# Kernel optimization log

Measured on AMD Instinct MI355X. Metric: run time of the kernel, lower is better.

The kernel has to match this reference:

```python
import jax, jax.numpy as jnp
import numpy as np

N_EMBD = 2048
N_HEAD = 16
N_KV_HEAD = 4
HD = N_EMBD // N_HEAD  # 128
B, T = 1, 4096
EPS = 1e-6


def apply_rope(x, cos, sin):
    # x: [B,T,H,hd]; cos/sin: [T,1,hd//2]
    hd = x.shape[-1] // 2
    x1, x2 = x[..., :hd], x[..., hd:]
    y1 = x1 * cos + x2 * sin
    y2 = x2 * cos - x1 * sin
    return jnp.concatenate((y1, y2), axis=-1).astype(x.dtype)


def rms_norm(x, eps=EPS):
    return x * jax.lax.rsqrt(jnp.mean(jnp.square(x), axis=-1, keepdims=True) + eps)


def setup_inputs() -> dict:
    key = jax.random.key(0)
    ks = jax.random.split(key, 7)
    s = 0.02
    return {
        "x": jax.random.normal(ks[0], (B, T, N_EMBD), dtype=jnp.float32),
        "cos": jax.random.normal(ks[1], (T, 1, HD // 2), dtype=jnp.float32),
        "sin": jax.random.normal(ks[2], (T, 1, HD // 2), dtype=jnp.float32),
        "wq": jax.random.normal(ks[3], (N_EMBD, N_HEAD * HD), dtype=jnp.float32) * s,
        "wk": jax.random.normal(ks[4], (N_EMBD, N_KV_HEAD * HD), dtype=jnp.float32) * s,
        "wv": jax.random.normal(ks[5], (N_EMBD, N_KV_HEAD * HD), dtype=jnp.float32) * s,
        "wo": jax.random.normal(ks[6], (N_EMBD, N_EMBD), dtype=jnp.float32) * s,
    }


def reference(x, cos, sin, wq, wk, wv, wo):
    Bb, Tt, C = x.shape
    q = (x @ wq).reshape(Bb, Tt, N_HEAD, HD)
    k = (x @ wk).reshape(Bb, Tt, N_KV_HEAD, HD)
    v = (x @ wv).reshape(Bb, Tt, N_KV_HEAD, HD)
    q = rms_norm(apply_rope(q, cos, sin))
    k = rms_norm(apply_rope(k, cos, sin))
    g = N_HEAD // N_KV_HEAD
    if g > 1:
        k = jnp.repeat(k, g, axis=2)  # [B,T,H,hd]
        v = jnp.repeat(v, g, axis=2)
    scale = 1.0 / jnp.sqrt(jnp.float32(HD))
    # scores: [B,H,T,S]
    scores = jnp.einsum("bthd,bshd->bhts", q, k) * scale
    causal = jnp.tril(jnp.ones((Tt, Tt), dtype=bool))
    scores = jnp.where(causal, scores, jnp.finfo(scores.dtype).min)
    attn = jax.nn.softmax(scores, axis=-1)
    y = jnp.einsum("bhts,bshd->bthd", attn, v).reshape(Bb, Tt, C)
    return y @ wo
```

## Files before the change

kernel.cpp:

```cpp
#include <hip/hip_runtime.h>

#define T_SEQ 4096
#define C_EMB 2048
#define NH 16
#define NKV 4
#define HD 128

typedef short bf16x8 __attribute__((ext_vector_type(8)));
typedef float f32x4 __attribute__((ext_vector_type(4)));
typedef unsigned short u16x4 __attribute__((ext_vector_type(4)));

__device__ inline unsigned short f2bf(float f) {
    unsigned int u = __float_as_uint(f);
    unsigned int r = (u + 0x7FFFu + ((u >> 16) & 1u)) >> 16;
    return (unsigned short)r;
}

__device__ __forceinline__ void async_cp16(const unsigned short* g, unsigned short* l) {
    __builtin_amdgcn_global_load_lds((const __attribute__((address_space(1))) unsigned int*)g,
                                     (__attribute__((address_space(3))) unsigned int*)l,
                                     16, 0, 0);
}

__global__ __launch_bounds__(256) void cvt_bf16(const float* __restrict__ in,
                                                unsigned short* __restrict__ out, int n) {
    int i = (blockIdx.x * 256 + threadIdx.x) * 4;
    if (i >= n) return;
    float4 f = *(const float4*)(&in[i]);
    u16x4 o;
    o.x = f2bf(f.x); o.y = f2bf(f.y); o.z = f2bf(f.z); o.w = f2bf(f.w);
    *(u16x4*)(&out[i]) = o;
}

__global__ __launch_bounds__(256) void transpose_all(const float* __restrict__ wq,
                                                     const float* __restrict__ wk,
                                                     const float* __restrict__ wv,
                                                     const float* __restrict__ wo,
                                                     unsigned short* __restrict__ wqkvT,
                                                     unsigned short* __restrict__ woT) {
    __shared__ float tile[32][33];
    int z = blockIdx.z;
    const float* in;
    unsigned short* out;
    int ld_in;
    if (z == 0)      { in = wq; out = wqkvT;                         ld_in = 2048; }
    else if (z == 1) { in = wk; out = wqkvT + (size_t)2048 * 2048;   ld_in = 512;  }
    else if (z == 2) { in = wv; out = wqkvT + (size_t)2560 * 2048;   ld_in = 512;  }
    else             { in = wo; out = woT;                           ld_in = 2048; }
    if ((z == 1 || z == 2) && blockIdx.x >= 16) return;

    int x = blockIdx.x * 32 + threadIdx.x;
    for (int i = threadIdx.y; i < 32; i += 8) {
        int y = blockIdx.y * 32 + i;
        tile[i][threadIdx.x] = in[(size_t)y * ld_in + x];
    }
    __syncthreads();
    int xo = blockIdx.y * 32 + threadIdx.x;
    for (int i = threadIdx.y; i < 32; i += 8) {
        int yo = blockIdx.x * 32 + i;
        out[(size_t)yo * 2048 + xo] = f2bf(tile[threadIdx.x][i]);
    }
}

__global__ __launch_bounds__(256, 3) void gemm_qkv(const unsigned short* __restrict__ A,
                                                   const unsigned short* __restrict__ Bt,
                                                   const float* __restrict__ cosb,
                                                   const float* __restrict__ sinb,
                                                   unsigned short* __restrict__ Qn,
                                                   unsigned short* __restrict__ Kn,
                                                   unsigned short* __restrict__ Vt) {
    __shared__ __align__(16) unsigned short As[3][128 * 32];
    __shared__ __align__(16) unsigned short Bs[3][128 * 32];
    const int K = 2048;
    int t = threadIdx.x;
    int w = t >> 6, lane = t & 63;
    int ln = lane & 15, q = lane >> 4;
    int wm = w * 32;

    int d = blockIdx.y * 24 + blockIdx.x;
    int xcd = d & 7, l = d >> 3;
    int lx = l % 12, ly = l / 12;
    int bx = (xcd & 1) * 12 + lx;
    int by = (xcd >> 1) * 8 + ly;
    int m0 = by * 128, n0 = bx * 128;

    f32x4 acc[2][8] = {};

    int r0 = t >> 2, c0 = (t & 3) ^ ((t >> 4) & 3);
    int L1 = 256 + t;
    int r1 = L1 >> 2, c1 = (L1 & 3) ^ ((L1 >> 4) & 3);
    const unsigned short* a0 = &A[(size_t)(m0 + r0) * K + c0 * 8];
    const unsigned short* a1 = &A[(size_t)(m0 + r1) * K + c1 * 8];
    const unsigned short* b0 = &Bt[(size_t)(n0 + r0) * K + c0 * 8];
    const unsigned short* b1 = &Bt[(size_t)(n0 + r1) * K + c1 * 8];

    auto stage = [&](int b, int k0) {
        async_cp16(a0 + k0, &As[b][w * 512]);
        async_cp16(a1 + k0, &As[b][2048 + w * 512]);
        async_cp16(b0 + k0, &Bs[b][w * 512]);
        async_cp16(b1 + k0, &Bs[b][2048 + w * 512]);
    };

    stage(0, 0);
    stage(1, 32);

    int bc = 0;
    for (int it = 0; it < 64; ++it) {
        if (it < 63) asm volatile("s_waitcnt vmcnt(4)" ::: "memory");
        else         asm volatile("s_waitcnt vmcnt(0)" ::: "memory");
        __builtin_amdgcn_s_barrier();
        __builtin_amdgcn_sched_barrier(0);
        if (it < 62) {
            int bn = bc + 2; if (bn >= 3) bn -= 3;
            stage(bn, (it + 2) * 32);
        }
        int cs = (q ^ ((ln >> 2) & 3)) * 8;
        bf16x8 af[2], bfr[8];
#pragma unroll
        for (int i = 0; i < 2; ++i) af[i] = *(const bf16x8*)(&As[bc][(wm + i * 16 + ln) * 32 + cs]);
#pragma unroll
        for (int j = 0; j < 8; ++j) bfr[j] = *(const bf16x8*)(&Bs[bc][(j * 16 + ln) * 32 + cs]);
#pragma unroll
        for (int i = 0; i < 2; ++i)
#pragma unroll
            for (int j = 0; j < 8; ++j)
                acc[i][j] = __builtin_amdgcn_mfma_f32_16x16x32_bf16(af[i], bfr[j], acc[i][j], 0, 0, 0);
        bc = (bc == 2) ? 0 : bc + 1;
    }

    if (n0 < 2560) {
        bool isQ = (n0 < 2048);
        int h = isQ ? (n0 >> 7) : ((n0 - 2048) >> 7);
#pragma unroll
        for (int i = 0; i < 2; ++i)
#pragma unroll
            for (int r = 0; r < 4; ++r) {
                int row = m0 + wm + i * 16 + q * 4 + r;
                float y1[4], y2[4];
                float ss = 0.0f;
#pragma unroll
                for (int j = 0; j < 4; ++j) {
                    float a = acc[i][j][r];
                    float b = acc[i][j + 4][r];
                    float cc = cosb[row * 64 + j * 16 + ln];
                    float sv = sinb[row * 64 + j * 16 + ln];
                    y1[j] = a * cc + b * sv;
                    y2[j] = b * cc - a * sv;
                    ss += y1[j] * y1[j] + y2[j] * y2[j];
                }
                ss += __shfl_xor(ss, 1);
                ss += __shfl_xor(ss, 2);
                ss += __shfl_xor(ss, 4);
                ss += __shfl_xor(ss, 8);
                float rv = rsqrtf(ss * (1.0f / 128.0f) + 1e-6f);
                if (isQ) {
                    float s = rv * (0.08838834764831845f * 1.4426950408889634f);
                    unsigned short* ob = Qn + (size_t)row * 2048 + h * 128;
#pragma unroll
                    for (int j = 0; j < 4; ++j) {
                        ob[j * 16 + ln] = f2bf(y1[j] * s);
                        ob[64 + j * 16 + ln] = f2bf(y2[j] * s);
                    }
                } else {
                    unsigned short* ob = Kn + (size_t)row * 512 + h * 128;
#pragma unroll
                    for (int j = 0; j < 4; ++j) {
                        ob[j * 16 + ln] = f2bf(y1[j] * rv);
                        ob[64 + j * 16 + ln] = f2bf(y2[j] * rv);
                    }
                }
            }
    } else {
        int v0 = n0 - 2560;
        unsigned short* sm = &As[0][0];
#pragma unroll
        for (int half = 0; half < 2; ++half) {
            __syncthreads();
#pragma unroll
            for (int i = 0; i < 2; ++i)
#pragma unroll
                for (int jj = 0; jj < 4; ++jj) {
                    int j = half * 4 + jj;
                    int cc = jj * 16 + ln;
                    int rr = wm + i * 16 + q * 4;
                    u16x4 pk;
                    pk.x = f2bf(acc[i][j][0]); pk.y = f2bf(acc[i][j][1]);
                    pk.z = f2bf(acc[i][j][2]); pk.w = f2bf(acc[i][j][3]);
                    *(u16x4*)(&sm[cc * 136 + rr]) = pk;
                }
            __syncthreads();
            int vtr = t >> 2, mseg = (t & 3) * 32;
            unsigned short* dst = Vt + (size_t)(v0 + half * 64 + vtr) * 4096 + m0 + mseg;
            const unsigned short* src = &sm[vtr * 136 + mseg];
            *(int4*)(dst)      = *(const int4*)(src);
            *(int4*)(dst + 8)  = *(const int4*)(src + 8);
            *(int4*)(dst + 16) = *(const int4*)(src + 16);
            *(int4*)(dst + 24) = *(const int4*)(src + 24);
        }
    }
}

__global__ __launch_bounds__(512, 2) void gemm_bt_256(const unsigned short* __restrict__ A,
                                                      const unsigned short* __restrict__ Bt,
                                                      float* __restrict__ C, int M, int N, int K) {
    __shared__ __align__(16) unsigned short As[2][256 * 64];
    __shared__ __align__(16) unsigned short Bs[2][256 * 64];
    int t = threadIdx.x;
    int w = t >> 6, lane = t & 63;
    int ln = lane & 15, q = lane >> 4;
    int wr = w >> 2, wc = w & 3;
    int m0 = blockIdx.y * 256, n0 = blockIdx.x * 256;

    f32x4 acc[8][4] = {};

    const unsigned short* ab[4];
    const unsigned short* bb[4];
#pragma unroll
    for (int s = 0; s < 4; ++s) {
        int L = s * 512 + t;
        int r = L >> 3;
        int c = (L & 7) ^ (r & 7);
        ab[s] = &A[(size_t)(m0 + r) * K + c * 8];
        bb[s] = &Bt[(size_t)(n0 + r) * K + c * 8];
    }

    auto stage = [&](int b, int k0) {
#pragma unroll
        for (int s = 0; s < 4; ++s) {
            async_cp16(ab[s] + k0, &As[b][s * 4096 + w * 512]);
            async_cp16(bb[s] + k0, &Bs[b][s * 4096 + w * 512]);
        }
    };

    stage(0, 0);
    asm volatile("s_waitcnt vmcnt(0)" ::: "memory");
    __builtin_amdgcn_s_barrier();

    int buf = 0;
    for (int it = 0; it < 32; ++it) {
        if (it < 31) stage(buf ^ 1, (it + 1) * 64);
#pragma unroll
        for (int kk = 0; kk < 2; ++kk) {
            bf16x8 bfr[4];
#pragma unroll
            for (int j = 0; j < 4; ++j) {
                int row = wc * 64 + j * 16 + ln;
                bfr[j] = *(const bf16x8*)(&Bs[buf][row * 64 + (((kk * 4 + q) ^ (row & 7)) * 8)]);
            }
#pragma unroll
            for (int i = 0; i < 8; ++i) {
                int row = wr * 128 + i * 16 + ln;
                bf16x8 a = *(const bf16x8*)(&As[buf][row * 64 + (((kk * 4 + q) ^ (row & 7)) * 8)]);
#pragma unroll
                for (int j = 0; j < 4; ++j)
                    acc[i][j] = __builtin_amdgcn_mfma_f32_16x16x32_bf16(a, bfr[j], acc[i][j], 0, 0, 0);
            }
        }
        asm volatile("s_waitcnt vmcnt(0)" ::: "memory");
        __builtin_amdgcn_s_barrier();
        buf ^= 1;
    }

#pragma unroll
    for (int i = 0; i < 8; ++i)
#pragma unroll
        for (int j = 0; j < 4; ++j)
#pragma unroll
            for (int r = 0; r < 4; ++r) {
                int row = m0 + wr * 128 + i * 16 + q * 4 + r;
                int col = n0 + wc * 64 + j * 16 + ln;
                C[(size_t)row * N + col] = acc[i][j][r];
            }
}

__global__ __launch_bounds__(256) void flash_attn(const unsigned short* __restrict__ Qn,
                                                  const unsigned short* __restrict__ Kn,
                                                  const unsigned short* __restrict__ Vt,
                                                  unsigned short* __restrict__ Ao) {
    __shared__ __align__(16) unsigned short Ks[2][64 * 128];
    __shared__ __align__(16) unsigned short Vs[2][128 * 64];
    __shared__ __align__(16) unsigned short Pl[4][16 * 72];

    int pairi = blockIdx.x;
    int h = blockIdx.y;
    int kvh = h >> 2;
    int t = threadIdx.x;
    int w = t >> 6, lane = t & 63;
    int ln = lane & 15, q = lane >> 4;

    int nA = 64 - pairi;
    int bq = 63 - pairi;
    int wq0 = bq * 64 + w * 16;

    bf16x8 qf[4];
    {
        const unsigned short* qb = Qn + (size_t)(wq0 + ln) * 2048 + h * 128;
#pragma unroll
        for (int kc = 0; kc < 4; ++kc) qf[kc] = *(const bf16x8*)(qb + kc * 32 + q * 8);
    }

    f32x4 o[8] = {};
    f32x4 l_p = {0.f, 0.f, 0.f, 0.f};

    const unsigned short* kbase[4];
    const unsigned short* vbase[4];
#pragma unroll
    for (int s = 0; s < 4; ++s) {
        int L = s * 256 + t;
        int key = L >> 4;
        int ck = (L & 15) ^ (key & 15);
        kbase[s] = Kn + (size_t)key * 512 + kvh * 128 + ck * 8;
        int hd = L >> 3;
        int cv = (L & 7) ^ (hd & 7);
        vbase[s] = Vt + (size_t)(kvh * 128 + hd) * 4096 + cv * 8;
    }

#pragma unroll
    for (int s = 0; s < 4; ++s) async_cp16(kbase[s], &Ks[0][s * 2048 + w * 512]);
#pragma unroll
    for (int s = 0; s < 4; ++s) async_cp16(vbase[s], &Vs[0][s * 2048 + w * 512]);

    for (int it = 0; it < 65; ++it) {
        __syncthreads();

        int nxt = it + 1;
        if (nxt < 65) {
            int nkt = (nxt < nA) ? nxt * 64 : (nxt - nA) * 64;
            size_t koff = (size_t)nkt * 512;
            unsigned short* kd = Ks[nxt & 1];
            unsigned short* vd = Vs[nxt & 1];
#pragma unroll
            for (int s = 0; s < 4; ++s) async_cp16(kbase[s] + koff, kd + s * 2048 + w * 512);
#pragma unroll
            for (int s = 0; s < 4; ++s) async_cp16(vbase[s] + nkt, vd + s * 2048 + w * 512);
        }

        if (it == nA) {
#pragma unroll
            for (int r = 0; r < 4; ++r) {
                float lsum = l_p[r];
                lsum += __shfl_xor(lsum, 1);
                lsum += __shfl_xor(lsum, 2);
                lsum += __shfl_xor(lsum, 4);
                lsum += __shfl_xor(lsum, 8);
                float inv = 1.0f / lsum;
                int row = wq0 + q * 4 + r;
                unsigned short* ob = Ao + (size_t)row * 2048 + h * 128;
#pragma unroll
                for (int f = 0; f < 8; ++f) ob[f * 16 + ln] = f2bf(o[f][r] * inv);
            }
            bq = pairi;
            wq0 = bq * 64 + w * 16;
            const unsigned short* qb = Qn + (size_t)(wq0 + ln) * 2048 + h * 128;
#pragma unroll
            for (int kc = 0; kc < 4; ++kc) qf[kc] = *(const bf16x8*)(qb + kc * 32 + q * 8);
#pragma unroll
            for (int f = 0; f < 8; ++f) o[f] = (f32x4){0.f, 0.f, 0.f, 0.f};
            l_p = (f32x4){0.f, 0.f, 0.f, 0.f};
        }

        int kt0 = (it < nA) ? it * 64 : (it - nA) * 64;
        const unsigned short* kb = Ks[it & 1];
        const unsigned short* vb = Vs[it & 1];

        f32x4 sA[4] = {{-16.6f, -16.6f, -16.6f, -16.6f}, {-16.6f, -16.6f, -16.6f, -16.6f},
                       {-16.6f, -16.6f, -16.6f, -16.6f}, {-16.6f, -16.6f, -16.6f, -16.6f}};
        __builtin_amdgcn_s_setprio(1);
#pragma unroll
        for (int jt = 0; jt < 4; ++jt) {
            int key = jt * 16 + ln;
#pragma unroll
            for (int kc = 0; kc < 4; ++kc) {
                int cs = ((kc * 4 + q) ^ ln) * 8;
                bf16x8 kf = *(const bf16x8*)(&kb[key * 128 + cs]);
                sA[jt] = __builtin_amdgcn_mfma_f32_16x16x32_bf16(qf[kc], kf, sA[jt], 0, 0, 0);
            }
        }
        __builtin_amdgcn_s_setprio(0);
        if (kt0 + 63 > wq0) {
#pragma unroll
            for (int jt = 0; jt < 4; ++jt)
#pragma unroll
                for (int r = 0; r < 4; ++r) {
                    int key = kt0 + jt * 16 + ln;
                    int row = wq0 + q * 4 + r;
                    if (key > row) sA[jt][r] = -3e38f;
                }
        }
#pragma unroll
        for (int r = 0; r < 4; ++r) {
            int prow = (q * 4 + r) * 72;
#pragma unroll
            for (int jt = 0; jt < 4; ++jt) {
                float p = __builtin_amdgcn_exp2f(sA[jt][r]);
                Pl[w][prow + jt * 16 + ln] = (unsigned short)(__float_as_uint(p) >> 16);
                l_p[r] += p;
            }
        }

        __builtin_amdgcn_s_setprio(1);
#pragma unroll
        for (int ks = 0; ks < 2; ++ks) {
            bf16x8 pa = *(const bf16x8*)(&Pl[w][ln * 72 + ks * 32 + q * 8]);
            int cs = ((ks * 4 + q) ^ (ln & 7)) * 8;
#pragma unroll
            for (int f = 0; f < 8; ++f) {
                bf16x8 vf = *(const bf16x8*)(&vb[(f * 16 + ln) * 64 + cs]);
                o[f] = __builtin_amdgcn_mfma_f32_16x16x32_bf16(pa, vf, o[f], 0, 0, 0);
            }
        }
        __builtin_amdgcn_s_setprio(0);
    }
#pragma unroll
    for (int r = 0; r < 4; ++r) {
        float lsum = l_p[r];
        lsum += __shfl_xor(lsum, 1);
        lsum += __shfl_xor(lsum, 2);
        lsum += __shfl_xor(lsum, 4);
        lsum += __shfl_xor(lsum, 8);
        float inv = 1.0f / lsum;
        int row = wq0 + q * 4 + r;
        unsigned short* ob = Ao + (size_t)row * 2048 + h * 128;
#pragma unroll
        for (int f = 0; f < 8; ++f) ob[f * 16 + ln] = f2bf(o[f][r] * inv);
    }
}

extern "C" void kernel_launch(void* const* d_in, const int* in_sizes, int n_in,
                              void* d_out, int out_size, void* d_ws, size_t ws_size,
                              hipStream_t stream) {
    const float* x    = (const float*)d_in[0];
    const float* cosb = (const float*)d_in[1];
    const float* sinb = (const float*)d_in[2];
    const float* wq   = (const float*)d_in[3];
    const float* wk   = (const float*)d_in[4];
    const float* wv   = (const float*)d_in[5];
    const float* wo   = (const float*)d_in[6];
    float* out = (float*)d_out;

    char* ws = (char*)d_ws;
    unsigned short* xb    = (unsigned short*)ws;
    unsigned short* wqkvT = xb    + (size_t)4096 * 2048;
    unsigned short* woT   = wqkvT + (size_t)3072 * 2048;
    unsigned short* Qn    = woT   + (size_t)2048 * 2048;
    unsigned short* Kn    = Qn    + (size_t)4096 * 2048;
    unsigned short* Vt    = Kn    + (size_t)4096 * 512;
    unsigned short* Ao    = Vt    + (size_t)512 * 4096;

    cvt_bf16<<<(4096 * 2048 / 4 + 255) / 256, 256, 0, stream>>>(x, xb, 4096 * 2048);
    transpose_all<<<dim3(64, 64, 4), dim3(32, 8), 0, stream>>>(wq, wk, wv, wo, wqkvT, woT);
    gemm_qkv<<<dim3(24, 32), 256, 0, stream>>>(xb, wqkvT, cosb, sinb, Qn, Kn, Vt);
    flash_attn<<<dim3(32, 16), 256, 0, stream>>>(Qn, Kn, Vt, Ao);
    gemm_bt_256<<<dim3(8, 16), 512, 0, stream>>>(Ao, woT, out, 4096, 2048, 2048);
}
```

Before: 371.9 us.

## Restructure output projection GEMM into triple-buffered phased pipeline with smaller M tile

The output-projection GEMM drops from 256x256 to 128x256 tiles, doubling the grid from 128 to 256 blocks so more CUs are occupied. It replaces double buffering with a 3-stage LDS ring that prefetches two k-steps ahead. Each k-step is split into four MFMA phases, with async loads interleaved and s_setprio raised around the MFMA bursts. The cost is extra barriers per iteration and more total operand traffic from the smaller M tile. The vmcnt(6) counting also has to match the number of outstanding loads exactly.

```diff
diff --git a/kernel.cpp b/kernel.cpp
--- a/kernel.cpp
+++ b/kernel.cpp
@@ -200,74 +200,141 @@
     }
 }
 
-__global__ __launch_bounds__(512, 2) void gemm_bt_256(const unsigned short* __restrict__ A,
+__global__ __launch_bounds__(512, 2) void gemm_bt_8ph(const unsigned short* __restrict__ A,
                                                       const unsigned short* __restrict__ Bt,
                                                       float* __restrict__ C, int M, int N, int K) {
-    __shared__ __align__(16) unsigned short As[2][256 * 64];
-    __shared__ __align__(16) unsigned short Bs[2][256 * 64];
+    __shared__ __align__(16) unsigned short As[3][128 * 64];
+    __shared__ __align__(16) unsigned short Bs[3][256 * 64];
     int t = threadIdx.x;
     int w = t >> 6, lane = t & 63;
     int ln = lane & 15, q = lane >> 4;
     int wr = w >> 2, wc = w & 3;
-    int m0 = blockIdx.y * 256, n0 = blockIdx.x * 256;
-
-    f32x4 acc[8][4] = {};
-
-    const unsigned short* ab[4];
+    int m0 = blockIdx.y * 128, n0 = blockIdx.x * 256;
+
+    f32x4 acc[4][4] = {};
+
+    const unsigned short* ab[2];
     const unsigned short* bb[4];
+#pragma unroll
+    for (int s = 0; s < 2; ++s) {
+        int L = s * 512 + t;
+        int r = L >> 3, c = (L & 7) ^ (r & 7);
+        ab[s] = &A[(size_t)(m0 + r) * K + c * 8];
+    }
 #pragma unroll
     for (int s = 0; s < 4; ++s) {
         int L = s * 512 + t;
-        int r = L >> 3;
-        int c = (L & 7) ^ (r & 7);
-        ab[s] = &A[(size_t)(m0 + r) * K + c * 8];
+        int r = L >> 3, c = (L & 7) ^ (r & 7);
         bb[s] = &Bt[(size_t)(n0 + r) * K + c * 8];
     }
 
-    auto stage = [&](int b, int k0) {
-#pragma unroll
-        for (int s = 0; s < 4; ++s) {
-            async_cp16(ab[s] + k0, &As[b][s * 4096 + w * 512]);
-            async_cp16(bb[s] + k0, &Bs[b][s * 4096 + w * 512]);
-        }
+    auto stageA = [&](int b, int k0) {
+        async_cp16(ab[0] + k0, &As[b][w * 512]);
+        async_cp16(ab[1] + k0, &As[b][4096 + w * 512]);
     };
-
-    stage(0, 0);
-    asm volatile("s_waitcnt vmcnt(0)" ::: "memory");
-    __builtin_amdgcn_s_barrier();
-
-    int buf = 0;
+    auto stageB01 = [&](int b, int k0) {
+        async_cp16(bb[0] + k0, &Bs[b][w * 512]);
+        async_cp16(bb[1] + k0, &Bs[b][4096 + w * 512]);
+    };
+    auto stageB23 = [&](int b, int k0) {
+        async_cp16(bb[2] + k0, &Bs[b][8192 + w * 512]);
+        async_cp16(bb[3] + k0, &Bs[b][12288 + w * 512]);
+    };
+
+    stageA(0, 0); stageB01(0, 0); stageB23(0, 0);
+    stageA(1, 64); stageB01(1, 64); stageB23(1, 64);
+
+    int bc = 0;
     for (int it = 0; it < 32; ++it) {
-        if (it < 31) stage(buf ^ 1, (it + 1) * 64);
-#pragma unroll
-        for (int kk = 0; kk < 2; ++kk) {
-            bf16x8 bfr[4];
-#pragma unroll
-            for (int j = 0; j < 4; ++j) {
-                int row = wc * 64 + j * 16 + ln;
-                bfr[j] = *(const bf16x8*)(&Bs[buf][row * 64 + (((kk * 4 + q) ^ (row & 7)) * 8)]);
-            }
-#pragma unroll
-            for (int i = 0; i < 8; ++i) {
-                int row = wr * 128 + i * 16 + ln;
-                bf16x8 a = *(const bf16x8*)(&As[buf][row * 64 + (((kk * 4 + q) ^ (row & 7)) * 8)]);
-#pragma unroll
-                for (int j = 0; j < 4; ++j)
-                    acc[i][j] = __builtin_amdgcn_mfma_f32_16x16x32_bf16(a, bfr[j], acc[i][j], 0, 0, 0);
-            }
-        }
-        asm volatile("s_waitcnt vmcnt(0)" ::: "memory");
+        if (it < 31) asm volatile("s_waitcnt vmcnt(6)" ::: "memory");
+        else         asm volatile("s_waitcnt vmcnt(0)" ::: "memory");
         __builtin_amdgcn_s_barrier();
-        buf ^= 1;
-    }
-
-#pragma unroll
-    for (int i = 0; i < 8; ++i)
+
+        int bn = bc + 2; if (bn >= 3) bn -= 3;
+        int kn = (it + 2) * 64;
+        bool doStage = (it < 30);
+        const unsigned short* as = &As[bc][0];
+        const unsigned short* bs = &Bs[bc][0];
+        bf16x8 af[4], bfr[4];
+
+#pragma unroll
+        for (int i = 0; i < 4; ++i) {
+            int row = wr * 64 + i * 16 + ln;
+            af[i] = *(const bf16x8*)(&as[row * 64 + ((q ^ (row & 7)) * 8)]);
+        }
+#pragma unroll
+        for (int j = 0; j < 2; ++j) {
+            int row = wc * 64 + j * 16 + ln;
+            bfr[j] = *(const bf16x8*)(&bs[row * 64 + ((q ^ (row & 7)) * 8)]);
+        }
+        if (doStage) stageA(bn, kn);
+        __builtin_amdgcn_s_setprio(1);
+#pragma unroll
+        for (int i = 0; i < 4; ++i)
+#pragma unroll
+            for (int j = 0; j < 2; ++j)
+                acc[i][j] = __builtin_amdgcn_mfma_f32_16x16x32_bf16(af[i], bfr[j], acc[i][j], 0, 0, 0);
+        __builtin_amdgcn_s_setprio(0);
+        __builtin_amdgcn_s_barrier();
+
+#pragma unroll
+        for (int j = 2; j < 4; ++j) {
+            int row = wc * 64 + j * 16 + ln;
+            bfr[j] = *(const bf16x8*)(&bs[row * 64 + ((q ^ (row & 7)) * 8)]);
+        }
+        if (doStage) stageB01(bn, kn);
+        __builtin_amdgcn_s_setprio(1);
+#pragma unroll
+        for (int i = 0; i < 4; ++i)
+#pragma unroll
+            for (int j = 2; j < 4; ++j)
+                acc[i][j] = __builtin_amdgcn_mfma_f32_16x16x32_bf16(af[i], bfr[j], acc[i][j], 0, 0, 0);
+        __builtin_amdgcn_s_setprio(0);
+        __builtin_amdgcn_s_barrier();
+
+#pragma unroll
+        for (int i = 0; i < 4; ++i) {
+            int row = wr * 64 + i * 16 + ln;
+            af[i] = *(const bf16x8*)(&as[row * 64 + (((4 + q) ^ (row & 7)) * 8)]);
+        }
+#pragma unroll
+        for (int j = 0; j < 2; ++j) {
+            int row = wc * 64 + j * 16 + ln;
+            bfr[j] = *(const bf16x8*)(&bs[row * 64 + (((4 + q) ^ (row & 7)) * 8)]);
+        }
+        if (doStage) stageB23(bn, kn);
+        __builtin_amdgcn_s_setprio(1);
+#pragma unroll
+        for (int i = 0; i < 4; ++i)
+#pragma unroll
+            for (int j = 0; j < 2; ++j)
+                acc[i][j] = __builtin_amdgcn_mfma_f32_16x16x32_bf16(af[i], bfr[j], acc[i][j], 0, 0, 0);
+        __builtin_amdgcn_s_setprio(0);
+        __builtin_amdgcn_s_barrier();
+
+#pragma unroll
+        for (int j = 2; j < 4; ++j) {
+            int row = wc * 64 + j * 16 + ln;
+            bfr[j] = *(const bf16x8*)(&bs[row * 64 + (((4 + q) ^ (row & 7)) * 8)]);
+        }
+        __builtin_amdgcn_s_setprio(1);
+#pragma unroll
+        for (int i = 0; i < 4; ++i)
+#pragma unroll
+            for (int j = 2; j < 4; ++j)
+                acc[i][j] = __builtin_amdgcn_mfma_f32_16x16x32_bf16(af[i], bfr[j], acc[i][j], 0, 0, 0);
+        __builtin_amdgcn_s_setprio(0);
+
+        bc = (bc == 2) ? 0 : bc + 1;
+    }
+
+#pragma unroll
+    for (int i = 0; i < 4; ++i)
 #pragma unroll
         for (int j = 0; j < 4; ++j)
 #pragma unroll
             for (int r = 0; r < 4; ++r) {
-                int row = m0 + wr * 128 + i * 16 + q * 4 + r;
+                int row = m0 + wr * 64 + i * 16 + q * 4 + r;
                 int col = n0 + wc * 64 + j * 16 + ln;
                 C[(size_t)row * N + col] = acc[i][j][r];
             }
@@ -451,5 +518,5 @@
     transpose_all<<<dim3(64, 64, 4), dim3(32, 8), 0, stream>>>(wq, wk, wv, wo, wqkvT, woT);
     gemm_qkv<<<dim3(24, 32), 256, 0, stream>>>(xb, wqkvT, cosb, sinb, Qn, Kn, Vt);
     flash_attn<<<dim3(32, 16), 256, 0, stream>>>(Qn, Kn, Vt, Ao);
-    gemm_bt_256<<<dim3(8, 16), 512, 0, stream>>>(Ao, woT, out, 4096, 2048, 2048);
-}
+    gemm_bt_8ph<<<dim3(8, 32), 512, 0, stream>>>(Ao, woT, out, 4096, 2048, 2048);
+}
```

After: 354.9 us. 4.6% less time.
